# Kernel tuning notes

Hardware: AMD Instinct MI355X
Metric: run time of the kernel (lower is better)

Reference implementation:

```python
import jax, jax.numpy as jnp
import numpy as np

NUM_NODES = 2048
NUM_UNITS = 64
INPUT_DIM = 2
MAX_K = 2  # max_diffusion_step


def setup_inputs() -> dict:
    key = jax.random.key(0)
    ks = jax.random.split(key, 8)
    B, N, U, D = 32, NUM_NODES, NUM_UNITS, INPUT_DIM
    C = D + U                      # input_size after concat = 66
    M = 2 * MAX_K + 1              # num_matrices = 5
    w_scale = 1.0 / np.sqrt(C * M)
    return {
        "inputs": jax.random.normal(ks[0], (B, N * D), dtype=jnp.float32),
        "hx": jax.random.normal(ks[1], (B, N * U), dtype=jnp.float32),
        # row-stochastic-ish random-walk supports (scaled so K hops stay bounded)
        "support0": jax.random.uniform(ks[2], (N, N), dtype=jnp.float32) / N,
        "support1": jax.random.uniform(ks[3], (N, N), dtype=jnp.float32) / N,
        "W_ru": jax.random.normal(ks[4], (C * M, 2 * U), dtype=jnp.float32) * w_scale,
        "b_ru": jnp.full((2 * U,), 1.0, dtype=jnp.float32),   # bias_start=1.0
        "W_c": jax.random.normal(ks[5], (C * M, U), dtype=jnp.float32) * w_scale,
        "b_c": jnp.zeros((U,), dtype=jnp.float32),            # bias_start=0.0
    }


def _gconv(inputs, state, supports, W, b, output_size):
    # inputs: [B, N*D], state: [B, N*U]
    B = inputs.shape[0]
    N = NUM_NODES
    x0 = jnp.concatenate(
        [inputs.reshape(B, N, -1), state.reshape(B, N, -1)], axis=2
    )  # [B, N, C]
    C = x0.shape[2]
    xs = [x0]
    for S in supports:  # Chebyshev-style diffusion per support
        x1 = jnp.einsum("nm,bmc->bnc", S, x0)
        xs.append(x1)
        xk1, xk2 = x1, x0
        for _ in range(2, MAX_K + 1):
            x2 = 2.0 * jnp.einsum("nm,bmc->bnc", S, xk1) - xk2
            xs.append(x2)
            xk1, xk2 = x2, xk1
    M = len(xs)  # num_matrices
    # stack on new leading axis then permute(1,2,3,0): feature-major, matrix-minor
    x = jnp.stack(xs, axis=0).transpose(1, 2, 3, 0).reshape(B * N, C * M)
    out = x @ W + b  # [B*N, output_size]
    return out.reshape(B, N * output_size)


def reference(inputs, hx, support0, support1, W_ru, b_ru, W_c, b_c):
    B = inputs.shape[0]
    N, U = NUM_NODES, NUM_UNITS
    supports = (support0, support1)
    value = jax.nn.sigmoid(_gconv(inputs, hx, supports, W_ru, b_ru, 2 * U))
    value = value.reshape(B, N, 2 * U)
    r = value[..., :U].reshape(B, N * U)
    u = value[..., U:].reshape(B, N * U)
    c = jnp.tanh(_gconv(inputs, r * hx, supports, W_c, b_c, U))
    new_state = u * hx + (1.0 - u) * c
    return new_state
```

## Files before the change

kernel.cpp:

```cpp
#include <hip/hip_runtime.h>
#include <hip/hip_bf16.h>
#include <cstdint>
#include <cstddef>

typedef unsigned short u16;
typedef unsigned char u8;
using f32x4 = __attribute__((ext_vector_type(4))) float;
using s16x8 = __attribute__((ext_vector_type(8))) short;
using s64x2 = __attribute__((ext_vector_type(2))) long;

#define NN 2048
#define BB 32
#define CC 66
#define JREAL 2112
#define JR 2176
#define KF 352
#define SROWS 65536

__device__ __forceinline__ int kperm(int k6) {
  return 16 * ((k6 >> 3) & 3) + 8 * (k6 >> 5) + (k6 & 7);
}

__device__ __forceinline__ float bf2f(u16 u) {
  union { uint32_t i; float f; } v; v.i = ((uint32_t)u) << 16; return v.f;
}
__device__ __forceinline__ u16 f2bf(float f) {
  union { float f; uint32_t i; } v; v.f = f;
  uint32_t x = v.i;
  x += 0x7fffu + ((x >> 16) & 1u);
  return (u16)(x >> 16);
}
__device__ __forceinline__ u8 f2e4m3(float x) {
  union { float f; uint32_t i; } v; v.f = x;
  uint32_t s = (v.i >> 24) & 0x80u;
  float a = fabsf(x);
  if (a >= 464.0f) return (u8)(s | 0x7Eu);
  if (a < 0.015625f) {
    int q = (int)rintf(a * 512.0f);
    return (u8)(s | (uint32_t)q);
  }
  union { float f; uint32_t i; } u; u.f = a;
  uint32_t lsb = (u.i >> 20) & 1u;
  u.i += 0x0007FFFFu + lsb;
  int e = (int)(u.i >> 23) - 127;
  uint32_t m = (u.i >> 20) & 7u;
  return (u8)(s | ((uint32_t)(e + 7) << 3) | m);
}

__device__ __forceinline__ void async_cp16(const u8* g, u8* l) {
  __builtin_amdgcn_global_load_lds(
      (const __attribute__((address_space(1))) unsigned int*)g,
      (__attribute__((address_space(3))) unsigned int*)l, 16, 0, 0);
}
__device__ __forceinline__ void async_cp16u(const u16* g, u16* l) {
  __builtin_amdgcn_global_load_lds(
      (const __attribute__((address_space(1))) unsigned int*)g,
      (__attribute__((address_space(3))) unsigned int*)l, 16, 0, 0);
}

template <int EPI>
__global__ __launch_bounds__(512, 2) void gemm_f8(
    const u8* __restrict__ A0, const u8* __restrict__ A1,
    const u8* __restrict__ A2, const u8* __restrict__ A3,
    const u8* __restrict__ B0, const u8* __restrict__ B1,
    const u8* __restrict__ B2, const u8* __restrict__ B3,
    void* __restrict__ C0, void* __restrict__ C1,
    void* __restrict__ C2, void* __restrict__ C3,
    int K, int lda, int ldb, int ldout, int mlimit)
{
  __shared__ u8 lds[3 * 25600];

  const int gx = gridDim.x, gy = gridDim.y;
  const int nwg = gx * gy * gridDim.z;
  const int orig = blockIdx.x + gx * (blockIdx.y + gy * blockIdx.z);
  const int cpx = nwg >> 3;
  const int swz = (orig & 7) * cpx + (orig >> 3);
  const int mb = swz % gx;
  const int t1 = swz / gx;
  const int nb = t1 % gy;
  const int zb = t1 / gy;

  const u8* A = (zb == 0) ? A0 : (zb == 1) ? A1 : (zb == 2) ? A2 : A3;
  const u8* B = (zb == 0) ? B0 : (zb == 1) ? B1 : (zb == 2) ? B2 : B3;
  void* Cv    = (zb == 0) ? C0 : (zb == 1) ? C1 : (zb == 2) ? C2 : C3;

  const int tid = threadIdx.x;
  const int wid = tid >> 6;
  const int lane = tid & 63;
  const int m0 = mb * 128;
  const int n0 = nb * 256;
  const int wm = (wid >> 2) * 64;
  const int wn = (wid & 3) * 64;

  const bool xtra = (EPI == 5) && (mb < 4);
  const int xrow0 = 2048 + mb * 16;
  const bool xw = xtra && (wid == 0);
  const bool xm = xtra && (wid < 4);

  const int srow = wid * 16 + (lane >> 2);
  const int sk   = ((lane & 3) ^ ((lane >> 3) & 3)) * 16;
  const u8* gA = A + (size_t)(m0 + srow) * lda + sk;
  const u8* gB = B + (size_t)(n0 + srow) * ldb + sk;
  const u8* gAx = A + (size_t)(xrow0 + (lane >> 2)) * lda + sk;
  u8* ldsA  = &lds[wid * 1024];
  u8* ldsB0 = &lds[8192 + wid * 1024];
  u8* ldsB1 = &lds[16384 + wid * 1024];
  u8* ldsAx = &lds[24576];

  const int r16 = lane & 15;
  const int hi = lane >> 4;
  const int rq = (r16 >> 1) & 3;
  const int goff = (hi ^ rq) * 16;
  const int abase = (wm + r16) * 64 + goff;
  const int bbase = 8192 + (wn + r16) * 64 + goff;
  const int xbase = 24576 + r16 * 64 + goff;

  f32x4 acc[4][4] = {};
  f32x4 accx[4] = {};
  const int nt = K >> 6;

#define STAGE_ALL(T_, SO_) { const int k0_ = (T_) * 64;                      \
    async_cp16(gA + k0_, ldsA + (SO_));                                      \
    async_cp16(gB + k0_, ldsB0 + (SO_));                                     \
    async_cp16(gB + (size_t)128 * ldb + k0_, ldsB1 + (SO_));                 \
    if (xw) async_cp16(gAx + k0_, ldsAx + (SO_)); }

  STAGE_ALL(0, 0);
  STAGE_ALL(1, 25600);
  if (xw) { asm volatile("s_waitcnt vmcnt(4)" ::: "memory"); }
  else    { asm volatile("s_waitcnt vmcnt(3)" ::: "memory"); }
  __builtin_amdgcn_s_barrier();

  int scur = 0;
  for (int t = 0; t < nt; ++t) {
    const int soff = scur * 25600;
    const bool more = (t + 2) < nt;
    int sst = scur + 2; if (sst >= 3) sst -= 3;
    const int so2 = sst * 25600;
    const int k2 = (t + 2) * 64;

    s64x2 af[4], bq0, bq1, axf;

#pragma unroll
    for (int mi = 0; mi < 4; ++mi)
      af[mi] = *(const s64x2*)&lds[soff + abase + mi * 1024];
    bq0 = *(const s64x2*)&lds[soff + bbase];
    bq1 = *(const s64x2*)&lds[soff + bbase + 1024];
    if (xm) axf = *(const s64x2*)&lds[soff + xbase];
    if (more) {
      async_cp16(gA + k2, ldsA + so2);
      async_cp16(gB + k2, ldsB0 + so2);
    }
    __builtin_amdgcn_s_barrier();
    asm volatile("s_waitcnt lgkmcnt(0)" ::: "memory");
    __builtin_amdgcn_s_setprio(1);
#pragma unroll
    for (int h = 0; h < 2; ++h) {
#pragma unroll
      for (int mi = 0; mi < 4; ++mi) {
        acc[mi][0] = __builtin_amdgcn_mfma_f32_16x16x32_fp8_fp8(
            af[mi][h], bq0[h], acc[mi][0], 0, 0, 0);
        acc[mi][1] = __builtin_amdgcn_mfma_f32_16x16x32_fp8_fp8(
            af[mi][h], bq1[h], acc[mi][1], 0, 0, 0);
      }
      if (xm) {
        accx[0] = __builtin_amdgcn_mfma_f32_16x16x32_fp8_fp8(
            axf[h], bq0[h], accx[0], 0, 0, 0);
        accx[1] = __builtin_amdgcn_mfma_f32_16x16x32_fp8_fp8(
            axf[h], bq1[h], accx[1], 0, 0, 0);
      }
    }
    __builtin_amdgcn_s_setprio(0);
    __builtin_amdgcn_s_barrier();

    bq0 = *(const s64x2*)&lds[soff + bbase + 2048];
    bq1 = *(const s64x2*)&lds[soff + bbase + 3072];
    if (more) {
      async_cp16(gB + (size_t)128 * ldb + k2, ldsB1 + so2);
      if (xw) async_cp16(gAx + k2, ldsAx + so2);
    }
    __builtin_amdgcn_s_barrier();
    asm volatile("s_waitcnt lgkmcnt(0)" ::: "memory");
    __builtin_amdgcn_s_setprio(1);
#pragma unroll
    for (int h = 0; h < 2; ++h) {
#pragma unroll
      for (int mi = 0; mi < 4; ++mi) {
        acc[mi][2] = __builtin_amdgcn_mfma_f32_16x16x32_fp8_fp8(
            af[mi][h], bq0[h], acc[mi][2], 0, 0, 0);
        acc[mi][3] = __builtin_amdgcn_mfma_f32_16x16x32_fp8_fp8(
            af[mi][h], bq1[h], acc[mi][3], 0, 0, 0);
      }
      if (xm) {
        accx[2] = __builtin_amdgcn_mfma_f32_16x16x32_fp8_fp8(
            axf[h], bq0[h], accx[2], 0, 0, 0);
        accx[3] = __builtin_amdgcn_mfma_f32_16x16x32_fp8_fp8(
            axf[h], bq1[h], accx[3], 0, 0, 0);
      }
    }
    __builtin_amdgcn_s_setprio(0);
    if (more) {
      if (xw) { asm volatile("s_waitcnt vmcnt(4)" ::: "memory"); }
      else    { asm volatile("s_waitcnt vmcnt(3)" ::: "memory"); }
    } else {
      asm volatile("s_waitcnt vmcnt(0)" ::: "memory");
    }
    __builtin_amdgcn_s_barrier();
    scur = (scur + 1 == 3) ? 0 : scur + 1;
  }
#undef STAGE_ALL

  const int lr = (lane >> 4) * 4;
  const int lc = lane & 15;

  if (EPI == 5) {
    u16* tl = (u16*)lds;
    u16* xc = (u16*)Cv;
    if (xm) {
#pragma unroll
      for (int ni = 0; ni < 4; ++ni) {
        const int ng = n0 + wn + ni * 16 + lc;
#pragma unroll
        for (int r = 0; r < 4; ++r) {
          const int c = xrow0 + lr + r - 2046;
          xc[((size_t)31 * NN + ng) * KF + (size_t)(zb + 1) * CC + c] =
              f2bf(accx[ni][r] * 0.00390625f);
        }
      }
    }
#pragma unroll
    for (int half = 0; half < 2; ++half) {
      __syncthreads();
      if ((wn >> 7) == half) {
#pragma unroll
        for (int mi = 0; mi < 4; ++mi)
#pragma unroll
          for (int ni = 0; ni < 4; ++ni) {
            const int np = (wn & 127) + ni * 16 + lc;
#pragma unroll
            for (int r = 0; r < 4; ++r) {
              const int j = wm + mi * 16 + lr + r;
              tl[np * 130 + j] = f2bf(acc[mi][ni][r] * 0.00390625f);
            }
          }
      }
      __syncthreads();
      for (int p = 0; p < 32; ++p) {
        const int idx = p * 512 + tid;
        const int jj = idx & 127;
        const int np = idx >> 7;
        const int j = m0 + jj;
        if (j < JREAL) {
          const int b = j / CC;
          const int c = j - b * CC;
          const int ng = n0 + half * 128 + np;
          xc[((size_t)b * NN + ng) * KF + (size_t)(zb + 1) * CC + c] =
              tl[np * 130 + jj];
        }
      }
    }
  } else {
#pragma unroll
    for (int mi = 0; mi < 4; ++mi)
#pragma unroll
      for (int ni = 0; ni < 4; ++ni) {
        const int colg = n0 + wn + ni * 16 + lc;
#pragma unroll
        for (int r = 0; r < 4; ++r) {
          const int rowg = m0 + wm + mi * 16 + lr + r;
          if (rowg < mlimit) {
            if (EPI == 0) {
              ((u16*)Cv)[(size_t)rowg * ldout + colg] =
                  f2bf(acc[mi][ni][r] * 0.00390625f);
            } else {
              float v = acc[mi][ni][r] * 0.0078125f -
                        ((rowg == colg) ? 256.0f : 0.0f);
              const int cpk = (colg & ~63) + kperm(colg & 63);
              ((u8*)Cv)[(size_t)rowg * ldout + cpk] = f2e4m3(v);
            }
          }
        }
      }
  }
}

__global__ __launch_bounds__(512, 2) void gemm_f8T(
    const u8* __restrict__ A0, const u8* __restrict__ A1,
    const u8* __restrict__ B0, const u8* __restrict__ B1,
    u8* __restrict__ C0, u8* __restrict__ C1,
    int K, int lda, int ldb, int ldout)
{
  __shared__ u8 lds[3 * 16384];

  const int gx = gridDim.x, gy = gridDim.y;
  const int nwg = gx * gy * gridDim.z;
  const int orig = blockIdx.x + gx * (blockIdx.y + gy * blockIdx.z);
  const int cpx = nwg >> 3;
  const int swz = (orig & 7) * cpx + (orig >> 3);
  const int mb = swz % gx;
  const int t1 = swz / gx;
  const int nb = t1 % gy;
  const int zb = t1 / gy;

  const u8* A = zb ? A1 : A0;
  const u8* B = zb ? B1 : B0;
  u8* C = zb ? C1 : C0;

  const int tid = threadIdx.x;
  const int wid = tid >> 6;
  const int lane = tid & 63;
  const int m0 = mb * 128;
  const int n0 = nb * 128;
  const int wm = (wid >> 2) * 64;
  const int wn = (wid & 3) * 32;

  const int srow = wid * 16 + (lane >> 2);
  const int sk   = ((lane & 3) ^ ((lane >> 3) & 3)) * 16;
  const u8* gA = A + (size_t)(m0 + srow) * lda + sk;
  const u8* gB = B + (size_t)(n0 + srow) * ldb + sk;
  u8* ldsA = &lds[wid * 1024];
  u8* ldsB = &lds[8192 + wid * 1024];

  const int r16 = lane & 15;
  const int hi = lane >> 4;
  const int rq = (r16 >> 1) & 3;
  const int goff = (hi ^ rq) * 16;
  const int abase = (wm + r16) * 64 + goff;
  const int bbase = 8192 + (wn + r16) * 64 + goff;

  f32x4 acc[4][2] = {};
  const int nt = K >> 6;

#define STAGE(T_, SO_) { const int k0_ = (T_) * 64;                          \
    async_cp16(gA + k0_, ldsA + (SO_));                                      \
    async_cp16(gB + k0_, ldsB + (SO_)); }

  STAGE(0, 0);
  STAGE(1, 16384);
  asm volatile("s_waitcnt vmcnt(2)" ::: "memory");
  __builtin_amdgcn_s_barrier();

  int scur = 0;
  for (int t = 0; t < nt; ++t) {
    const int soff = scur * 16384;
    const bool more = (t + 2) < nt;
    int sst = scur + 2; if (sst >= 3) sst -= 3;
    const int so2 = sst * 16384;
    const int k2 = (t + 2) * 64;

    s64x2 af[4], bq;

#pragma unroll
    for (int mi = 0; mi < 4; ++mi)
      af[mi] = *(const s64x2*)&lds[soff + abase + mi * 1024];
    bq = *(const s64x2*)&lds[soff + bbase];
    if (more) async_cp16(gA + k2, ldsA + so2);
    __builtin_amdgcn_s_barrier();
    asm volatile("s_waitcnt lgkmcnt(0)" ::: "memory");
    __builtin_amdgcn_s_setprio(1);
#pragma unroll
    for (int h = 0; h < 2; ++h)
#pragma unroll
      for (int mi = 0; mi < 4; ++mi)
        acc[mi][0] = __builtin_amdgcn_mfma_f32_16x16x32_fp8_fp8(
            af[mi][h], bq[h], acc[mi][0], 0, 0, 0);
    __builtin_amdgcn_s_setprio(0);
    __builtin_amdgcn_s_barrier();

    bq = *(const s64x2*)&lds[soff + bbase + 1024];
    if (more) async_cp16(gB + k2, ldsB + so2);
    __builtin_amdgcn_s_barrier();
    asm volatile("s_waitcnt lgkmcnt(0)" ::: "memory");
    __builtin_amdgcn_s_setprio(1);
#pragma unroll
    for (int h = 0; h < 2; ++h)
#pragma unroll
      for (int mi = 0; mi < 4; ++mi)
        acc[mi][1] = __builtin_amdgcn_mfma_f32_16x16x32_fp8_fp8(
            af[mi][h], bq[h], acc[mi][1], 0, 0, 0);
    __builtin_amdgcn_s_setprio(0);
    if (more) { asm volatile("s_waitcnt vmcnt(2)" ::: "memory"); }
    else      { asm volatile("s_waitcnt vmcnt(0)" ::: "memory"); }
    __builtin_amdgcn_s_barrier();
    scur = (scur + 1 == 3) ? 0 : scur + 1;
  }
#undef STAGE

  const int lr = (lane >> 4) * 4;
  const int lc = lane & 15;
#pragma unroll
  for (int mi = 0; mi < 4; ++mi)
#pragma unroll
    for (int ni = 0; ni < 2; ++ni) {
      const int colg = n0 + wn + ni * 16 + lc;
      const int cpk = (colg & ~63) + kperm(colg & 63);
#pragma unroll
      for (int r = 0; r < 4; ++r) {
        const int rowg = m0 + wm + mi * 16 + lr + r;
        float v = acc[mi][ni][r] * 0.0078125f -
                  ((rowg == colg) ? 256.0f : 0.0f);
        C[(size_t)rowg * ldout + cpk] = f2e4m3(v);
      }
    }
}

template <int EPI>
__global__ __launch_bounds__(256) void gemm_dense(
    const u16* __restrict__ A, const u16* __restrict__ B, u16* __restrict__ C,
    const float* __restrict__ bias,
    const u16* __restrict__ rug, const float* __restrict__ hxg,
    float* __restrict__ outg,
    int K, int lda, int ldb, int ldout, int nstore)
{
  __shared__ u16 At[128 * 32];
  __shared__ u16 Bt[128 * 32];
  const int nwg = gridDim.x;
  const int orig = blockIdx.x;
  const int cpx = nwg >> 3;
  const int swz = (orig & 7) * cpx + (orig >> 3);
  const int mb = swz;

  const int tid = threadIdx.x;
  const int wid = tid >> 6;
  const int lane = tid & 63;
  const int m0 = mb * 128;
  const int wm = (wid >> 1) * 64;
  const int wn = (wid & 1) * 64;
  const int rA = lane >> 2;
  const int kA = ((lane & 3) ^ ((lane >> 3) & 3)) * 8;

  f32x4 acc[4][4] = {};

  const int c0 = wid * 2, c1 = wid * 2 + 1;
  const u16* gA0 = A + (size_t)(m0 + c0 * 16 + rA) * lda + kA;
  const u16* gA1 = A + (size_t)(m0 + c1 * 16 + rA) * lda + kA;
  const u16* gB0 = B + (size_t)(c0 * 16 + rA) * ldb + kA;
  const u16* gB1 = B + (size_t)(c1 * 16 + rA) * ldb + kA;

  for (int k0 = 0; k0 < K; k0 += 32) {
    async_cp16u(gA0 + k0, &At[c0 * 512]);
    async_cp16u(gA1 + k0, &At[c1 * 512]);
    async_cp16u(gB0 + k0, &Bt[c0 * 512]);
    async_cp16u(gB1 + k0, &Bt[c1 * 512]);
    __syncthreads();
    s16x8 af[4], bfr[4];
    const int r16 = lane & 15;
    const int cswz = ((lane >> 4) ^ ((r16 >> 1) & 3)) << 3;
#pragma unroll
    for (int mi = 0; mi < 4; ++mi)
      af[mi] = *(const s16x8*)&At[(wm + mi * 16 + r16) * 32 + cswz];
#pragma unroll
    for (int ni = 0; ni < 4; ++ni)
      bfr[ni] = *(const s16x8*)&Bt[(wn + ni * 16 + r16) * 32 + cswz];
#pragma unroll
    for (int mi = 0; mi < 4; ++mi)
#pragma unroll
      for (int ni = 0; ni < 4; ++ni)
        acc[mi][ni] = __builtin_amdgcn_mfma_f32_16x16x32_bf16(af[mi], bfr[ni], acc[mi][ni], 0, 0, 0);
    __syncthreads();
  }

  const int lr = (lane >> 4) * 4;
  const int lc = lane & 15;
#pragma unroll
  for (int mi = 0; mi < 4; ++mi) {
#pragma unroll
    for (int ni = 0; ni < 4; ++ni) {
      const int colg = wn + ni * 16 + lc;
#pragma unroll
      for (int r = 0; r < 4; ++r) {
        const int rowg = m0 + wm + mi * 16 + lr + r;
        float v = acc[mi][ni][r];
        if (EPI == 2) {
          v += bias[colg]; v = 1.0f / (1.0f + __expf(-v));
          if (colg < nstore)
            C[(size_t)rowg * ldout + colg] = f2bf(v);
        }
        if (EPI == 3) {
          if (colg < nstore) {
            v += bias[colg]; v = tanhf(v);
            const size_t s = (size_t)rowg;
            const float ug = bf2f(rug[s * 128 + 64 + colg]);
            const float h  = hxg[s * 64 + colg];
            outg[s * 64 + colg] = ug * h + (1.0f - ug) * v;
          }
        }
      }
    }
  }
}

__global__ __launch_bounds__(256) void cvt_S(const float* __restrict__ Sa,
                                             const float* __restrict__ Sb,
                                             u8* __restrict__ Sha, u8* __restrict__ Shb,
                                             u8* __restrict__ Sta, u8* __restrict__ Stb) {
  __shared__ u8 tile[64 * 68];
  const float* S = blockIdx.z ? Sb : Sa;
  u8* Sh = blockIdx.z ? Shb : Sha;
  u8* St = blockIdx.z ? Stb : Sta;
  const int c0 = blockIdx.x * 64;
  const int r0 = blockIdx.y * 64;
  const int t = threadIdx.x;
#pragma unroll
  for (int p = 0; p < 4; ++p) {
    const int idx = p * 256 + t;
    const int r = idx >> 4;
    const int c4 = (idx & 15) * 4;
    float4 v = *reinterpret_cast<const float4*>(S + (size_t)(r0 + r) * NN + c0 + c4);
    union { u8 b[4]; uint32_t w; } o;
    o.b[0] = f2e4m3(v.x * 256.0f); o.b[1] = f2e4m3(v.y * 256.0f);
    o.b[2] = f2e4m3(v.z * 256.0f); o.b[3] = f2e4m3(v.w * 256.0f);
    *reinterpret_cast<uint32_t*>(Sh + (size_t)(r0 + r) * NN + c0 + kperm(c4)) = o.w;
    *reinterpret_cast<uint32_t*>(&tile[r * 68 + c4]) = o.w;
  }
  __syncthreads();
  const int cc = t >> 2;
#pragma unroll
  for (int half = 0; half < 2; ++half) {
    const int j = (t & 3) * 2 + half;
    union { u8 b[8]; uint64_t w; } buf;
#pragma unroll
    for (int i = 0; i < 8; ++i) buf.b[i] = tile[(j * 8 + i) * 68 + cc];
    const int npos = 16 * (j & 3) + 8 * (j >> 2);
    *reinterpret_cast<uint64_t*>(St + (size_t)(c0 + cc) * NN + r0 + npos) = buf.w;
  }
}

__global__ __launch_bounds__(256) void build_wt(const float* __restrict__ W,
                                                u16* __restrict__ Wt, int ocols) {
  int t = blockIdx.x * 256 + threadIdx.x;
  if (t >= 128 * KF) return;
  int o = t / KF, kf = t - o * KF;
  float v = 0.0f;
  if (kf < 330 && o < ocols) {
    int m = kf / CC, c = kf - m * CC;
    v = W[(size_t)(c * 5 + m) * ocols + o];
  }
  Wt[t] = f2bf(v);
}

__global__ __launch_bounds__(256) void pack_x0(const float* __restrict__ inputs,
                                               const float* __restrict__ hx,
                                               const u16* __restrict__ ru,
                                               u8* __restrict__ X0t,
                                               u16* __restrict__ xcat, int useR) {
  __shared__ u16 tile[128 * 76];
  const int n0 = blockIdx.x * 128;
  const int b = blockIdx.y;
  const int t = threadIdx.x;
#pragma unroll
  for (int p = 0; p < 8; ++p) {
    const int idx = p * 256 + t;
    const int n = idx >> 4;
    const int u4 = (idx & 15) * 4;
    float4 v = *reinterpret_cast<const float4*>(
        hx + (size_t)b * (NN * 64) + (size_t)(n0 + n) * 64 + u4);
    if (useR) {
      ushort4 rv = *reinterpret_cast<const ushort4*>(
          ru + ((size_t)b * NN + n0 + n) * 128 + u4);
      v.x *= bf2f(rv.x); v.y *= bf2f(rv.y); v.z *= bf2f(rv.z); v.w *= bf2f(rv.w);
    }
    ushort4 o;
    o.x = f2bf(v.x); o.y = f2bf(v.y); o.z = f2bf(v.z); o.w = f2bf(v.w);
    *reinterpret_cast<ushort4*>(&tile[n * 76 + u4]) = o;
  }
  __syncthreads();
#pragma unroll
  for (int p = 0; p < 33; ++p) {
    const int idx = p * 256 + t;
    const int c = idx >> 7;
    const int n = idx & 127;
    float val;
    if (c < 2) val = inputs[(size_t)b * (NN * 2) + (size_t)(n0 + n) * 2 + c];
    else       val = bf2f(tile[n * 76 + (c - 2)]);
    const int np = (n & ~63) + kperm(n & 63);
    X0t[(size_t)(b * CC + c) * NN + n0 + np] = f2e4m3(val);
  }
#pragma unroll
  for (int p = 0; p < 17; ++p) {
    const int idx = p * 256 + t;
    if (idx < 128 * 33) {
      const int n = idx / 33;
      const int pr = idx - n * 33;
      const int col = pr * 2;
      u16 v0, v1;
      if (col == 0) {
        v0 = f2bf(inputs[(size_t)b * (NN * 2) + (size_t)(n0 + n) * 2 + 0]);
        v1 = f2bf(inputs[(size_t)b * (NN * 2) + (size_t)(n0 + n) * 2 + 1]);
      } else {
        v0 = tile[n * 76 + (col - 2)];
        v1 = tile[n * 76 + (col - 1)];
      }
      ushort2 o2; o2.x = v0; o2.y = v1;
      *reinterpret_cast<ushort2*>(
          xcat + ((size_t)b * NN + n0 + n) * KF + col) = o2;
    }
  }
}

extern "C" void kernel_launch(void* const* d_in, const int* in_sizes, int n_in,
                              void* d_out, int out_size, void* d_ws, size_t ws_size,
                              hipStream_t stream) {
  const float* inputs = (const float*)d_in[0];
  const float* hx     = (const float*)d_in[1];
  const float* S0     = (const float*)d_in[2];
  const float* S1     = (const float*)d_in[3];
  const float* Wru    = (const float*)d_in[4];
  const float* bru    = (const float*)d_in[5];
  const float* Wc     = (const float*)d_in[6];
  const float* bc     = (const float*)d_in[7];
  float* out = (float*)d_out;

  u8* ws8 = (u8*)d_ws;
  u8* S0h = ws8;
  u8* S1h = S0h + (size_t)NN * NN;
  u8* X0t = S1h + (size_t)NN * NN;
  u16* xcat = (u16*)(X0t + (size_t)JR * NN);
  u16* Wtru = xcat + (size_t)SROWS * KF;
  u16* Wtc  = Wtru + (size_t)128 * KF;
  u16* ru   = Wtc + (size_t)128 * KF;
  u8* S0t = (u8*)xcat;
  u8* S1t = S0t + (size_t)NN * NN;
  u8* T0 = (u8*)d_out;
  u8* T1 = T0 + (size_t)NN * NN;

  dim3 b256(256);
  dim3 b512(512);
  cvt_S<<<dim3(NN / 64, NN / 64, 2), b256, 0, stream>>>(S0, S1, S0h, S1h, S0t, S1t);
  build_wt<<<dim3((128 * KF + 255) / 256), b256, 0, stream>>>(Wru, Wtru, 128);
  build_wt<<<dim3((128 * KF + 255) / 256), b256, 0, stream>>>(Wc, Wtc, 64);

  gemm_f8T<<<dim3(NN / 128, NN / 128, 2), b512, 0, stream>>>(
      S0h, S1h, S0t, S1t, T0, T1, NN, NN, NN, NN);

  const dim3 gdiff(16, NN / 256, 4);
  const dim3 gdense(SROWS / 128);
  const dim3 gpx0(NN / 128, BB);

  pack_x0<<<gpx0, b256, 0, stream>>>(inputs, hx, (const u16*)nullptr, X0t, xcat, 0);
  gemm_f8<5><<<gdiff, b512, 0, stream>>>(
      X0t, X0t, X0t, X0t,  S0h, T0, S1h, T1,
      (void*)xcat, (void*)xcat, (void*)xcat, (void*)xcat,
      NN, NN, NN, KF, JREAL);
  gemm_dense<2><<<gdense, b256, 0, stream>>>(
      xcat, Wtru, ru, bru, (const u16*)nullptr, (const float*)nullptr,
      (float*)nullptr, KF, KF, KF, 128, 128);

  pack_x0<<<gpx0, b256, 0, stream>>>(inputs, hx, ru, X0t, xcat, 1);
  gemm_f8<5><<<gdiff, b512, 0, stream>>>(
      X0t, X0t, X0t, X0t,  S0h, T0, S1h, T1,
      (void*)xcat, (void*)xcat, (void*)xcat, (void*)xcat,
      NN, NN, NN, KF, JREAL);
  gemm_dense<3><<<gdense, b256, 0, stream>>>(
      xcat, Wtc, (u16*)nullptr, bc, ru, hx, out, KF, KF, KF, 64, 64);
}
```

Before: 270.8 us.

## Double diffusion GEMM M-tile to 256 and simplify gemm_f8T pipeline loop

The diffusion GEMM now computes 256x256 tiles per workgroup with an 8x4 accumulator array per wave, staged in four phases that reuse B fragments across A slices. This halves the grid and is meant to cut redundant global/LDS traffic per FLOP. The epilogue transposes through a larger LDS buffer and drops the row guard. The gemm_f8T main loop issues both next-stage copies up front and merges its two MFMA phases, removing intermediate barriers. The larger LDS footprint and doubled accumulators likely limit occupancy to one block per CU.

```diff
diff --git a/kernel.cpp b/kernel.cpp
--- a/kernel.cpp
+++ b/kernel.cpp
@@ -68,7 +68,7 @@
     void* __restrict__ C2, void* __restrict__ C3,
     int K, int lda, int ldb, int ldout, int mlimit)
 {
-  __shared__ u8 lds[3 * 25600];
+  __shared__ u8 lds[3 * 33792];
 
   const int gx = gridDim.x, gy = gridDim.y;
   const int nwg = gx * gy * gridDim.z;
@@ -87,9 +87,9 @@
   const int tid = threadIdx.x;
   const int wid = tid >> 6;
   const int lane = tid & 63;
-  const int m0 = mb * 128;
+  const int m0 = mb * 256;
   const int n0 = nb * 256;
-  const int wm = (wid >> 2) * 64;
+  const int wm = (wid >> 2) * 128;
   const int wn = (wid & 3) * 64;
 
   const bool xtra = (EPI == 5) && (mb < 4);
@@ -103,112 +103,150 @@
   const u8* gB = B + (size_t)(n0 + srow) * ldb + sk;
   const u8* gAx = A + (size_t)(xrow0 + (lane >> 2)) * lda + sk;
   u8* ldsA  = &lds[wid * 1024];
-  u8* ldsB0 = &lds[8192 + wid * 1024];
-  u8* ldsB1 = &lds[16384 + wid * 1024];
-  u8* ldsAx = &lds[24576];
+  u8* ldsB  = &lds[16384 + wid * 1024];
+  u8* ldsAx = &lds[32768];
 
   const int r16 = lane & 15;
   const int hi = lane >> 4;
   const int rq = (r16 >> 1) & 3;
   const int goff = (hi ^ rq) * 16;
   const int abase = (wm + r16) * 64 + goff;
-  const int bbase = 8192 + (wn + r16) * 64 + goff;
-  const int xbase = 24576 + r16 * 64 + goff;
-
-  f32x4 acc[4][4] = {};
+  const int bbase = 16384 + (wn + r16) * 64 + goff;
+  const int xbase = 32768 + r16 * 64 + goff;
+
+  f32x4 acc[8][4] = {};
   f32x4 accx[4] = {};
   const int nt = K >> 6;
 
+#define SLOT 33792
 #define STAGE_ALL(T_, SO_) { const int k0_ = (T_) * 64;                      \
     async_cp16(gA + k0_, ldsA + (SO_));                                      \
-    async_cp16(gB + k0_, ldsB0 + (SO_));                                     \
-    async_cp16(gB + (size_t)128 * ldb + k0_, ldsB1 + (SO_));                 \
+    async_cp16(gA + (size_t)128 * lda + k0_, ldsA + 8192 + (SO_));           \
+    async_cp16(gB + k0_, ldsB + (SO_));                                      \
+    async_cp16(gB + (size_t)128 * ldb + k0_, ldsB + 8192 + (SO_));           \
     if (xw) async_cp16(gAx + k0_, ldsAx + (SO_)); }
 
   STAGE_ALL(0, 0);
-  STAGE_ALL(1, 25600);
-  if (xw) { asm volatile("s_waitcnt vmcnt(4)" ::: "memory"); }
-  else    { asm volatile("s_waitcnt vmcnt(3)" ::: "memory"); }
+  STAGE_ALL(1, SLOT);
+  if (xw) { asm volatile("s_waitcnt vmcnt(5)" ::: "memory"); }
+  else    { asm volatile("s_waitcnt vmcnt(4)" ::: "memory"); }
   __builtin_amdgcn_s_barrier();
 
   int scur = 0;
   for (int t = 0; t < nt; ++t) {
-    const int soff = scur * 25600;
+    const int soff = scur * SLOT;
     const bool more = (t + 2) < nt;
     int sst = scur + 2; if (sst >= 3) sst -= 3;
-    const int so2 = sst * 25600;
+    const int so2 = sst * SLOT;
     const int k2 = (t + 2) * 64;
 
-    s64x2 af[4], bq0, bq1, axf;
-
-#pragma unroll
-    for (int mi = 0; mi < 4; ++mi)
-      af[mi] = *(const s64x2*)&lds[soff + abase + mi * 1024];
-    bq0 = *(const s64x2*)&lds[soff + bbase];
-    bq1 = *(const s64x2*)&lds[soff + bbase + 1024];
-    if (xm) axf = *(const s64x2*)&lds[soff + xbase];
-    if (more) {
-      async_cp16(gA + k2, ldsA + so2);
-      async_cp16(gB + k2, ldsB0 + so2);
-    }
-    __builtin_amdgcn_s_barrier();
-    asm volatile("s_waitcnt lgkmcnt(0)" ::: "memory");
-    __builtin_amdgcn_s_setprio(1);
-#pragma unroll
-    for (int h = 0; h < 2; ++h) {
-#pragma unroll
-      for (int mi = 0; mi < 4; ++mi) {
-        acc[mi][0] = __builtin_amdgcn_mfma_f32_16x16x32_fp8_fp8(
-            af[mi][h], bq0[h], acc[mi][0], 0, 0, 0);
-        acc[mi][1] = __builtin_amdgcn_mfma_f32_16x16x32_fp8_fp8(
-            af[mi][h], bq1[h], acc[mi][1], 0, 0, 0);
-      }
-      if (xm) {
-        accx[0] = __builtin_amdgcn_mfma_f32_16x16x32_fp8_fp8(
-            axf[h], bq0[h], accx[0], 0, 0, 0);
-        accx[1] = __builtin_amdgcn_mfma_f32_16x16x32_fp8_fp8(
-            axf[h], bq1[h], accx[1], 0, 0, 0);
-      }
-    }
-    __builtin_amdgcn_s_setprio(0);
-    __builtin_amdgcn_s_barrier();
-
-    bq0 = *(const s64x2*)&lds[soff + bbase + 2048];
-    bq1 = *(const s64x2*)&lds[soff + bbase + 3072];
-    if (more) {
-      async_cp16(gB + (size_t)128 * ldb + k2, ldsB1 + so2);
-      if (xw) async_cp16(gAx + k2, ldsAx + so2);
-    }
-    __builtin_amdgcn_s_barrier();
-    asm volatile("s_waitcnt lgkmcnt(0)" ::: "memory");
-    __builtin_amdgcn_s_setprio(1);
-#pragma unroll
-    for (int h = 0; h < 2; ++h) {
-#pragma unroll
-      for (int mi = 0; mi < 4; ++mi) {
-        acc[mi][2] = __builtin_amdgcn_mfma_f32_16x16x32_fp8_fp8(
-            af[mi][h], bq0[h], acc[mi][2], 0, 0, 0);
-        acc[mi][3] = __builtin_amdgcn_mfma_f32_16x16x32_fp8_fp8(
-            af[mi][h], bq1[h], acc[mi][3], 0, 0, 0);
-      }
-      if (xm) {
-        accx[2] = __builtin_amdgcn_mfma_f32_16x16x32_fp8_fp8(
-            axf[h], bq0[h], accx[2], 0, 0, 0);
-        accx[3] = __builtin_amdgcn_mfma_f32_16x16x32_fp8_fp8(
-            axf[h], bq1[h], accx[3], 0, 0, 0);
-      }
-    }
-    __builtin_amdgcn_s_setprio(0);
-    if (more) {
-      if (xw) { asm volatile("s_waitcnt vmcnt(4)" ::: "memory"); }
-      else    { asm volatile("s_waitcnt vmcnt(3)" ::: "memory"); }
-    } else {
-      asm volatile("s_waitcnt vmcnt(0)" ::: "memory");
-    }
-    __builtin_amdgcn_s_barrier();
+    s64x2 bq[4], axf;
+
+    {
+      s64x2 a0 = *(const s64x2*)&lds[soff + abase];
+      s64x2 a1 = *(const s64x2*)&lds[soff + abase + 1024];
+#pragma unroll
+      for (int ni = 0; ni < 4; ++ni)
+        bq[ni] = *(const s64x2*)&lds[soff + bbase + ni * 1024];
+      if (xm) axf = *(const s64x2*)&lds[soff + xbase];
+      if (more) async_cp16(gA + k2, ldsA + so2);
+      __builtin_amdgcn_s_barrier();
+      asm volatile("s_waitcnt lgkmcnt(0)" ::: "memory");
+      __builtin_amdgcn_s_setprio(1);
+#pragma unroll
+      for (int h = 0; h < 2; ++h) {
+#pragma unroll
+        for (int ni = 0; ni < 4; ++ni) {
+          acc[0][ni] = __builtin_amdgcn_mfma_f32_16x16x32_fp8_fp8(
+              a0[h], bq[ni][h], acc[0][ni], 0, 0, 0);
+          acc[1][ni] = __builtin_amdgcn_mfma_f32_16x16x32_fp8_fp8(
+              a1[h], bq[ni][h], acc[1][ni], 0, 0, 0);
+        }
+        if (xm) accx[0] = __builtin_amdgcn_mfma_f32_16x16x32_fp8_fp8(
+            axf[h], bq[0][h], accx[0], 0, 0, 0);
+      }
+      __builtin_amdgcn_s_setprio(0);
+      __builtin_amdgcn_s_barrier();
+    }
+    {
+      s64x2 a0 = *(const s64x2*)&lds[soff + abase + 2 * 1024];
+      s64x2 a1 = *(const s64x2*)&lds[soff + abase + 3 * 1024];
+      if (more) async_cp16(gA + (size_t)128 * lda + k2, ldsA + 8192 + so2);
+      __builtin_amdgcn_s_barrier();
+      asm volatile("s_waitcnt lgkmcnt(0)" ::: "memory");
+      __builtin_amdgcn_s_setprio(1);
+#pragma unroll
+      for (int h = 0; h < 2; ++h) {
+#pragma unroll
+        for (int ni = 0; ni < 4; ++ni) {
+          acc[2][ni] = __builtin_amdgcn_mfma_f32_16x16x32_fp8_fp8(
+              a0[h], bq[ni][h], acc[2][ni], 0, 0, 0);
+          acc[3][ni] = __builtin_amdgcn_mfma_f32_16x16x32_fp8_fp8(
+              a1[h], bq[ni][h], acc[3][ni], 0, 0, 0);
+        }
+        if (xm) accx[1] = __builtin_amdgcn_mfma_f32_16x16x32_fp8_fp8(
+            axf[h], bq[1][h], accx[1], 0, 0, 0);
+      }
+      __builtin_amdgcn_s_setprio(0);
+      __builtin_amdgcn_s_barrier();
+    }
+    {
+      s64x2 a0 = *(const s64x2*)&lds[soff + abase + 4 * 1024];
+      s64x2 a1 = *(const s64x2*)&lds[soff + abase + 5 * 1024];
+      if (more) async_cp16(gB + k2, ldsB + so2);
+      __builtin_amdgcn_s_barrier();
+      asm volatile("s_waitcnt lgkmcnt(0)" ::: "memory");
+      __builtin_amdgcn_s_setprio(1);
+#pragma unroll
+      for (int h = 0; h < 2; ++h) {
+#pragma unroll
+        for (int ni = 0; ni < 4; ++ni) {
+          acc[4][ni] = __builtin_amdgcn_mfma_f32_16x16x32_fp8_fp8(
+              a0[h], bq[ni][h], acc[4][ni], 0, 0, 0);
+          acc[5][ni] = __builtin_amdgcn_mfma_f32_16x16x32_fp8_fp8(
+              a1[h], bq[ni][h], acc[5][ni], 0, 0, 0);
+        }
+        if (xm) accx[2] = __builtin_amdgcn_mfma_f32_16x16x32_fp8_fp8(
+            axf[h], bq[2][h], accx[2], 0, 0, 0);
+      }
+      __builtin_amdgcn_s_setprio(0);
+      __builtin_amdgcn_s_barrier();
+    }
+    {
+      s64x2 a0 = *(const s64x2*)&lds[soff + abase + 6 * 1024];
+      s64x2 a1 = *(const s64x2*)&lds[soff + abase + 7 * 1024];
+      if (more) {
+        async_cp16(gB + (size_t)128 * ldb + k2, ldsB + 8192 + so2);
+        if (xw) async_cp16(gAx + k2, ldsAx + so2);
+      }
+      __builtin_amdgcn_s_barrier();
+      asm volatile("s_waitcnt lgkmcnt(0)" ::: "memory");
+      __builtin_amdgcn_s_setprio(1);
+#pragma unroll
+      for (int h = 0; h < 2; ++h) {
+#pragma unroll
+        for (int ni = 0; ni < 4; ++ni) {
+          acc[6][ni] = __builtin_amdgcn_mfma_f32_16x16x32_fp8_fp8(
+              a0[h], bq[ni][h], acc[6][ni], 0, 0, 0);
+          acc[7][ni] = __builtin_amdgcn_mfma_f32_16x16x32_fp8_fp8(
+              a1[h], bq[ni][h], acc[7][ni], 0, 0, 0);
+        }
+        if (xm) accx[3] = __builtin_amdgcn_mfma_f32_16x16x32_fp8_fp8(
+            axf[h], bq[3][h], accx[3], 0, 0, 0);
+      }
+      __builtin_amdgcn_s_setprio(0);
+      if (more) {
+        if (xw) { asm volatile("s_waitcnt vmcnt(5)" ::: "memory"); }
+        else    { asm volatile("s_waitcnt vmcnt(4)" ::: "memory"); }
+      } else {
+        asm volatile("s_waitcnt vmcnt(0)" ::: "memory");
+      }
+      __builtin_amdgcn_s_barrier();
+    }
     scur = (scur + 1 == 3) ? 0 : scur + 1;
   }
 #undef STAGE_ALL
+#undef SLOT
 
   const int lr = (lane >> 4) * 4;
   const int lc = lane & 15;
@@ -233,35 +271,33 @@
       __syncthreads();
       if ((wn >> 7) == half) {
 #pragma unroll
-        for (int mi = 0; mi < 4; ++mi)
+        for (int mi = 0; mi < 8; ++mi)
 #pragma unroll
           for (int ni = 0; ni < 4; ++ni) {
             const int np = (wn & 127) + ni * 16 + lc;
 #pragma unroll
             for (int r = 0; r < 4; ++r) {
               const int j = wm + mi * 16 + lr + r;
-              tl[np * 130 + j] = f2bf(acc[mi][ni][r] * 0.00390625f);
+              tl[np * 258 + j] = f2bf(acc[mi][ni][r] * 0.00390625f);
             }
           }
       }
       __syncthreads();
-      for (int p = 0; p < 32; ++p) {
+      for (int p = 0; p < 64; ++p) {
         const int idx = p * 512 + tid;
-        const int jj = idx & 127;
-        const int np = idx >> 7;
+        const int jj = idx & 255;
+        const int np = idx >> 8;
         const int j = m0 + jj;
-        if (j < JREAL) {
-          const int b = j / CC;
-          const int c = j - b * CC;
-          const int ng = n0 + half * 128 + np;
-          xc[((size_t)b * NN + ng) * KF + (size_t)(zb + 1) * CC + c] =
-              tl[np * 130 + jj];
-        }
+        const int b = j / CC;
+        const int c = j - b * CC;
+        const int ng = n0 + half * 128 + np;
+        xc[((size_t)b * NN + ng) * KF + (size_t)(zb + 1) * CC + c] =
+            tl[np * 258 + jj];
       }
     }
   } else {
 #pragma unroll
-    for (int mi = 0; mi < 4; ++mi)
+    for (int mi = 0; mi < 8; ++mi)
 #pragma unroll
       for (int ni = 0; ni < 4; ++ni) {
         const int colg = n0 + wn + ni * 16 + lc;
@@ -344,40 +380,26 @@
   for (int t = 0; t < nt; ++t) {
     const int soff = scur * 16384;
     const bool more = (t + 2) < nt;
-    int sst = scur + 2; if (sst >= 3) sst -= 3;
-    const int so2 = sst * 16384;
-    const int k2 = (t + 2) * 64;
-
-    s64x2 af[4], bq;
-
+    if (more) {
+      int sst = scur + 2; if (sst >= 3) sst -= 3;
+      STAGE(t + 2, sst * 16384);
+    }
+    s64x2 af[4], bfr[2];
 #pragma unroll
     for (int mi = 0; mi < 4; ++mi)
       af[mi] = *(const s64x2*)&lds[soff + abase + mi * 1024];
-    bq = *(const s64x2*)&lds[soff + bbase];
-    if (more) async_cp16(gA + k2, ldsA + so2);
-    __builtin_amdgcn_s_barrier();
-    asm volatile("s_waitcnt lgkmcnt(0)" ::: "memory");
+#pragma unroll
+    for (int ni = 0; ni < 2; ++ni)
+      bfr[ni] = *(const s64x2*)&lds[soff + bbase + ni * 1024];
     __builtin_amdgcn_s_setprio(1);
 #pragma unroll
     for (int h = 0; h < 2; ++h)
 #pragma unroll
       for (int mi = 0; mi < 4; ++mi)
-        acc[mi][0] = __builtin_amdgcn_mfma_f32_16x16x32_fp8_fp8(
-            af[mi][h], bq[h], acc[mi][0], 0, 0, 0);
-    __builtin_amdgcn_s_setprio(0);
-    __builtin_amdgcn_s_barrier();
-
-    bq = *(const s64x2*)&lds[soff + bbase + 1024];
-    if (more) async_cp16(gB + k2, ldsB + so2);
-    __builtin_amdgcn_s_barrier();
-    asm volatile("s_waitcnt lgkmcnt(0)" ::: "memory");
-    __builtin_amdgcn_s_setprio(1);
-#pragma unroll
-    for (int h = 0; h < 2; ++h)
-#pragma unroll
-      for (int mi = 0; mi < 4; ++mi)
-        acc[mi][1] = __builtin_amdgcn_mfma_f32_16x16x32_fp8_fp8(
-            af[mi][h], bq[h], acc[mi][1], 0, 0, 0);
+#pragma unroll
+        for (int ni = 0; ni < 2; ++ni)
+          acc[mi][ni] = __builtin_amdgcn_mfma_f32_16x16x32_fp8_fp8(
+              af[mi][h], bfr[ni][h], acc[mi][ni], 0, 0, 0);
     __builtin_amdgcn_s_setprio(0);
     if (more) { asm volatile("s_waitcnt vmcnt(2)" ::: "memory"); }
     else      { asm volatile("s_waitcnt vmcnt(0)" ::: "memory"); }
@@ -633,7 +655,7 @@
   gemm_f8T<<<dim3(NN / 128, NN / 128, 2), b512, 0, stream>>>(
       S0h, S1h, S0t, S1t, T0, T1, NN, NN, NN, NN);
 
-  const dim3 gdiff(16, NN / 256, 4);
+  const dim3 gdiff(8, 8, 4);
   const dim3 gdense(SROWS / 128);
   const dim3 gpx0(NN / 128, BB);
 
```

After: 250.2 us. -7.6%, faster.
